# Kernel optimization log

Measured on AMD Instinct MI355X. Metric: run time of the kernel, lower is better.

Reference implementation:

```python
import jax, jax.numpy as jnp
import numpy as np
from jax import lax


def setup_inputs() -> dict:
    key = jax.random.key(0)
    k1, k2 = jax.random.split(key)
    X = jax.random.normal(k1, (4, 32, 512, 512), dtype=jnp.float32)
    kernel = jax.random.uniform(k2, (5, 5), dtype=jnp.float32)  # torch.rand equivalent
    return {"X": X, "kernel": kernel, "stride": 1, "padding": 2}


def reference(X, kernel, stride, padding):
    # Original module: zero-pad, unfold k x k patches with given stride, and
    # compute sum(patch * kernel) for every (batch, channel, row, col) -- i.e.
    # a per-channel 2D correlation with a single shared [k, k] kernel.
    # Fold channels into the batch dim so one single-channel correlation
    # covers all of them (no cross-channel mixing in the original).
    B, C, H, W = X.shape
    k = kernel.shape[0]
    Xf = X.reshape(B * C, 1, H, W)
    out = lax.conv_general_dilated(
        Xf,
        kernel[None, None, :, :],  # OIHW = [1, 1, k, k]
        window_strides=(stride, stride),
        padding=[(padding, padding), (padding, padding)],
        dimension_numbers=("NCHW", "OIHW", "NCHW"),
    )  # lax conv is correlation (no kernel flip), matching the torch math
    _, _, Ho, Wo = out.shape
    return out.reshape(B, C, Ho, Wo)
```

## Files before the change

kernel.cpp:

```cpp
#include <hip/hip_runtime.h>

#define H 512
#define W 512
#define K 5
#define PAD 2
#define RPT 8

__global__ __launch_bounds__(256) void conv5x5_kernel(
    const float* __restrict__ X, const float* __restrict__ ker,
    float* __restrict__ out)
{
    const int x   = blockIdx.x * 64 + threadIdx.x;
    const int y0  = (blockIdx.y * 4 + threadIdx.y) * RPT;
    const int img = blockIdx.z;

    const float* Xp = X   + (size_t)img * H * W;
    float*       Op = out + (size_t)img * H * W;

    float k[K][K];
    #pragma unroll
    for (int i = 0; i < K; ++i)
        #pragma unroll
        for (int j = 0; j < K; ++j)
            k[i][j] = ker[i * K + j];

    float acc[RPT];
    #pragma unroll
    for (int i = 0; i < RPT; ++i) acc[i] = 0.f;

    bool okc[K];
    #pragma unroll
    for (int c = 0; c < K; ++c) {
        int xc = x - PAD + c;
        okc[c] = (xc >= 0) && (xc < W);
    }

    #pragma unroll
    for (int r = 0; r < RPT + K - 1; ++r) {
        const int yr  = y0 - PAD + r;
        const bool okr = (yr >= 0) && (yr < H);
        const float* rowp = Xp + (size_t)yr * W + (x - PAD);

        float v[K];
        #pragma unroll
        for (int c = 0; c < K; ++c)
            v[c] = (okr && okc[c]) ? rowp[c] : 0.f;

        #pragma unroll
        for (int o = 0; o < RPT; ++o) {
            const int kr = r - o;
            if (kr >= 0 && kr < K) {
                #pragma unroll
                for (int c = 0; c < K; ++c)
                    acc[o] = fmaf(v[c], k[kr][c], acc[o]);
            }
        }
    }

    #pragma unroll
    for (int o = 0; o < RPT; ++o)
        Op[(size_t)(y0 + o) * W + x] = acc[o];
}

extern "C" void kernel_launch(void* const* d_in, const int* in_sizes, int n_in,
                              void* d_out, int out_size, void* d_ws, size_t ws_size,
                              hipStream_t stream) {
    const float* X   = (const float*)d_in[0];
    const float* ker = (const float*)d_in[1];
    float* out = (float*)d_out;

    dim3 block(64, 4, 1);
    dim3 grid(W / 64, H / (4 * RPT), 4 * 32);
    hipLaunchKernelGGL(conv5x5_kernel, grid, block, 0, stream, X, ker, out);
}
```

Baseline: 241.0 us.

## Compute four output columns per thread with float4 loads and stores

Each thread now produces a 4-wide by 8-tall output tile. It loads three aligned float4 vectors per input row (left, middle, right) and reuses the eight values across the four columns, instead of doing five scalar loads per single column. Output is written with float4 stores, and the grid shrinks by four in x. This cuts load instruction count and redundant global/L1 traffic in a memory-bound stencil, at the cost of more registers (32 accumulators) and fewer threads in flight.

Measured after the change: 251.6 us. +4.4%, slower.

```diff
diff --git a/kernel.cpp b/kernel.cpp
--- a/kernel.cpp
+++ b/kernel.cpp
@@ -5,46 +5,51 @@
 #define K 5
 #define PAD 2
 #define RPT 8
+#define XPT 4
 
 __global__ __launch_bounds__(256) void conv5x5_kernel(
     const float* __restrict__ X, const float* __restrict__ ker,
     float* __restrict__ out)
 {
-    const int x   = blockIdx.x * 64 + threadIdx.x;
+    const int tx  = threadIdx.x;
+    const int xb  = (blockIdx.x * 64 + tx) * XPT;
     const int y0  = (blockIdx.y * 4 + threadIdx.y) * RPT;
     const int img = blockIdx.z;
 
     const float* Xp = X   + (size_t)img * H * W;
     float*       Op = out + (size_t)img * H * W;
 
-    float k[K][K];
+    float kk[K][K];
     #pragma unroll
     for (int i = 0; i < K; ++i)
         #pragma unroll
         for (int j = 0; j < K; ++j)
-            k[i][j] = ker[i * K + j];
+            kk[i][j] = ker[i * K + j];
 
-    float acc[RPT];
+    float acc[RPT][XPT];
     #pragma unroll
-    for (int i = 0; i < RPT; ++i) acc[i] = 0.f;
+    for (int o = 0; o < RPT; ++o)
+        #pragma unroll
+        for (int j = 0; j < XPT; ++j)
+            acc[o][j] = 0.f;
 
-    bool okc[K];
-    #pragma unroll
-    for (int c = 0; c < K; ++c) {
-        int xc = x - PAD + c;
-        okc[c] = (xc >= 0) && (xc < W);
-    }
+    const bool okL = (xb - 4) >= 0;
+    const bool okR = (xb + 7) < W;
+    const int  q   = xb >> 2;
 
     #pragma unroll
     for (int r = 0; r < RPT + K - 1; ++r) {
-        const int yr  = y0 - PAD + r;
-        const bool okr = (yr >= 0) && (yr < H);
-        const float* rowp = Xp + (size_t)yr * W + (x - PAD);
-
-        float v[K];
-        #pragma unroll
-        for (int c = 0; c < K; ++c)
-            v[c] = (okr && okc[c]) ? rowp[c] : 0.f;
+        const int yr = y0 - PAD + r;
+        float4 Lv = {0.f, 0.f, 0.f, 0.f};
+        float4 Mv = {0.f, 0.f, 0.f, 0.f};
+        float4 Rv = {0.f, 0.f, 0.f, 0.f};
+        if (yr >= 0 && yr < H) {
+            const float4* rp = (const float4*)(Xp + (size_t)yr * W);
+            Mv = rp[q];
+            if (okL) Lv = rp[q - 1];
+            if (okR) Rv = rp[q + 1];
+        }
+        float v[8] = {Lv.z, Lv.w, Mv.x, Mv.y, Mv.z, Mv.w, Rv.x, Rv.y};
 
         #pragma unroll
         for (int o = 0; o < RPT; ++o) {
@@ -52,14 +57,18 @@
             if (kr >= 0 && kr < K) {
                 #pragma unroll
                 for (int c = 0; c < K; ++c)
-                    acc[o] = fmaf(v[c], k[kr][c], acc[o]);
+                    #pragma unroll
+                    for (int j = 0; j < XPT; ++j)
+                        acc[o][j] = fmaf(v[j + c], kk[kr][c], acc[o][j]);
             }
         }
     }
 
     #pragma unroll
-    for (int o = 0; o < RPT; ++o)
-        Op[(size_t)(y0 + o) * W + x] = acc[o];
+    for (int o = 0; o < RPT; ++o) {
+        float4 st = {acc[o][0], acc[o][1], acc[o][2], acc[o][3]};
+        *(float4*)(Op + (size_t)(y0 + o) * W + xb) = st;
+    }
 }
 
 extern "C" void kernel_launch(void* const* d_in, const int* in_sizes, int n_in,
@@ -70,6 +79,6 @@
     float* out = (float*)d_out;
 
     dim3 block(64, 4, 1);
-    dim3 grid(W / 64, H / (4 * RPT), 4 * 32);
+    dim3 grid(W / (64 * XPT), H / (4 * RPT), 4 * 32);
     hipLaunchKernelGGL(conv5x5_kernel, grid, block, 0, stream, X, ker, out);
 }
```
